# Kernel tuning notes

Measured on AMD Instinct MI355X. Metric: run time of the kernel, lower is better.

The kernel has to match this reference:

```python
import jax, jax.numpy as jnp
import numpy as np

T, B, D_IN, H = 256, 64, 512, 1024  # cell hidden = 2*H
D_OUT = 512
CH = 2 * H  # GRUCell hidden size


def setup_inputs() -> dict:
    key = jax.random.key(0)
    ks = jax.random.split(key, 12)
    s = 0.02
    x = jax.random.normal(ks[0], (T, B, D_IN), dtype=jnp.float32)
    # enc: Linear(D_IN, H)
    We = jax.random.normal(ks[1], (H, D_IN), dtype=jnp.float32) * s
    be = jnp.zeros((H,), dtype=jnp.float32)
    # GRUCell(H, CH): weight_ih [3*CH, H], weight_hh [3*CH, CH]
    Wih = jax.random.normal(ks[2], (3 * CH, H), dtype=jnp.float32) * s
    bih = jnp.zeros((3 * CH,), dtype=jnp.float32)
    Whh = jax.random.normal(ks[3], (3 * CH, CH), dtype=jnp.float32) * s
    bhh = jnp.zeros((3 * CH,), dtype=jnp.float32)
    # heads: Linear(H, D_OUT)
    Wmu = jax.random.normal(ks[4], (D_OUT, H), dtype=jnp.float32) * s
    bmu = jnp.zeros((D_OUT,), dtype=jnp.float32)
    Wsig = jax.random.normal(ks[5], (D_OUT, H), dtype=jnp.float32) * s
    bsig = jnp.zeros((D_OUT,), dtype=jnp.float32)
    return {"x": x, "We": We, "be": be, "Wih": Wih, "bih": bih,
            "Whh": Whh, "bhh": bhh, "Wmu": Wmu, "bmu": bmu,
            "Wsig": Wsig, "bsig": bsig}


def _forward(x, We, be, Wih, bih, Whh, bhh, Wmu, bmu, Wsig, bsig):
    # encode every timestep at once: [T,B,H]
    xe = jax.nn.elu(jnp.einsum('tbd,hd->tbh', x, We) + be)
    # precompute input-side gate preactivations: [T,B,3*CH]
    gx = jnp.einsum('tbh,gh->tbg', xe, Wih) + bih

    def step(h, gx_t):
        gh = h @ Whh.T + bhh                      # [B, 3*CH]
        xr, xz, xn = jnp.split(gx_t, 3, axis=-1)
        hr, hz, hn = jnp.split(gh, 3, axis=-1)
        r = jax.nn.sigmoid(xr + hr)
        z = jax.nn.sigmoid(xz + hz)
        n = jnp.tanh(xn + r * hn)
        h_new = (1.0 - z) * n + z * h
        return h_new, h_new

    h0 = jnp.zeros((x.shape[1], CH), dtype=x.dtype)
    _, hidden = jax.lax.scan(step, h0, gx)        # hidden: [T, B, 2H]

    h_mu, h_sig = jnp.split(hidden, 2, axis=2)    # each [T, B, H]
    mu = jax.nn.elu(jnp.einsum('tbh,oh->tbo', h_mu, Wmu) + bmu)
    sig = jax.nn.softplus(jnp.einsum('tbh,oh->tbo', h_sig, Wsig) + bsig) + 0.1
    return mu, sig, hidden


def reference(x, We, be, Wih, bih, Whh, bhh, Wmu, bmu, Wsig, bsig):
    # Returns (mu, sig, hidden); the torch module wraps (mu, sig) in Normal.
    return _forward(x, We, be, Wih, bih, Whh, bhh, Wmu, bmu, Wsig, bsig)
```

## Files before the change

kernel.cpp:

```cpp
#include <hip/hip_runtime.h>
#include <hip/hip_bf16.h>
#include <math.h>

#define T_STEPS 256
#define B_SZ 64
#define DIN 512
#define H_SZ 1024
#define CH_SZ 2048
#define G3 6144
#define DOUT 512
#define TB 16384

typedef __attribute__((ext_vector_type(4))) float f32x4;
typedef __attribute__((ext_vector_type(8))) short s16x8;
typedef __attribute__((ext_vector_type(4))) short s16x4;
typedef __attribute__((ext_vector_type(4))) unsigned u32x4;
typedef __attribute__((ext_vector_type(8))) __bf16 bf16x8;

__device__ __forceinline__ unsigned short f2bf(float f) {
  unsigned u = __builtin_bit_cast(unsigned, f);
  u += 0x7fffu + ((u >> 16) & 1u);
  return (unsigned short)(u >> 16);
}
__device__ __forceinline__ float bf2f(unsigned short h) {
  unsigned u = ((unsigned)h) << 16;
  return __builtin_bit_cast(float, u);
}
__device__ __forceinline__ f32x4 mfma16(s16x8 a, s16x8 b, f32x4 c) {
  return __builtin_amdgcn_mfma_f32_16x16x32_bf16(
      __builtin_bit_cast(bf16x8, a), __builtin_bit_cast(bf16x8, b), c, 0, 0, 0);
}
__device__ __forceinline__ s16x8 cvt8(f32x4 lo, f32x4 hi) {
  unsigned r0, r1, r2, r3;
  asm("v_cvt_pk_bf16_f32 %0, %1, %2" : "=v"(r0) : "v"(lo.x), "v"(lo.y));
  asm("v_cvt_pk_bf16_f32 %0, %1, %2" : "=v"(r1) : "v"(lo.z), "v"(lo.w));
  asm("v_cvt_pk_bf16_f32 %0, %1, %2" : "=v"(r2) : "v"(hi.x), "v"(hi.y));
  asm("v_cvt_pk_bf16_f32 %0, %1, %2" : "=v"(r3) : "v"(hi.z), "v"(hi.w));
  u32x4 p; p[0] = r0; p[1] = r1; p[2] = r2; p[3] = r3;
  return __builtin_bit_cast(s16x8, p);
}

template<bool AF32, int ACT, bool OBF>
__global__ __launch_bounds__(256, 2)
void gemm_bt(const void* __restrict__ Ap, long lda,
             const unsigned short* __restrict__ Bp,
             const float* __restrict__ bias,
             float* __restrict__ Cf, unsigned short* __restrict__ Cb, long ldc,
             int K)
{
  __shared__ unsigned short sA[128 * 40];
  __shared__ unsigned short sB[128 * 40];
  const int tid  = threadIdx.x;
  const int lane = tid & 63;
  const int wave = tid >> 6;
  const int wm = wave & 1, wn = wave >> 1;
  const int l16 = lane & 15, quad = lane >> 4;
  const long m0 = (long)blockIdx.x * 128;
  const long n0 = (long)blockIdx.y * 128;
  const int srow = tid >> 1;
  const int sseg = (tid & 1) << 4;

  f32x4 acc[4][4] = {};

  for (int k0 = 0; k0 < K; k0 += 32) {
    if constexpr (AF32) {
      const float* A = (const float*)Ap + (m0 + srow) * lda + (k0 + sseg);
      f32x4 v0 = *(const f32x4*)(A + 0);
      f32x4 v1 = *(const f32x4*)(A + 4);
      f32x4 v2 = *(const f32x4*)(A + 8);
      f32x4 v3 = *(const f32x4*)(A + 12);
      s16x8 p0, p1;
      p0[0] = (short)f2bf(v0.x); p0[1] = (short)f2bf(v0.y);
      p0[2] = (short)f2bf(v0.z); p0[3] = (short)f2bf(v0.w);
      p0[4] = (short)f2bf(v1.x); p0[5] = (short)f2bf(v1.y);
      p0[6] = (short)f2bf(v1.z); p0[7] = (short)f2bf(v1.w);
      p1[0] = (short)f2bf(v2.x); p1[1] = (short)f2bf(v2.y);
      p1[2] = (short)f2bf(v2.z); p1[3] = (short)f2bf(v2.w);
      p1[4] = (short)f2bf(v3.x); p1[5] = (short)f2bf(v3.y);
      p1[6] = (short)f2bf(v3.z); p1[7] = (short)f2bf(v3.w);
      *(s16x8*)&sA[srow * 40 + sseg]     = p0;
      *(s16x8*)&sA[srow * 40 + sseg + 8] = p1;
    } else {
      const unsigned short* A = (const unsigned short*)Ap + (m0 + srow) * lda + (k0 + sseg);
      *(s16x8*)&sA[srow * 40 + sseg]     = *(const s16x8*)(A);
      *(s16x8*)&sA[srow * 40 + sseg + 8] = *(const s16x8*)(A + 8);
    }
    {
      const unsigned short* Bq = Bp + (n0 + srow) * (long)K + (k0 + sseg);
      *(s16x8*)&sB[srow * 40 + sseg]     = *(const s16x8*)(Bq);
      *(s16x8*)&sB[srow * 40 + sseg + 8] = *(const s16x8*)(Bq + 8);
    }
    __syncthreads();
    s16x8 af[4], bfr[4];
#pragma unroll
    for (int i = 0; i < 4; ++i) {
      af[i]  = *(const s16x8*)&sA[(wm * 64 + i * 16 + l16) * 40 + quad * 8];
      bfr[i] = *(const s16x8*)&sB[(wn * 64 + i * 16 + l16) * 40 + quad * 8];
    }
#pragma unroll
    for (int mi = 0; mi < 4; ++mi)
#pragma unroll
      for (int ni = 0; ni < 4; ++ni)
        acc[mi][ni] = mfma16(af[mi], bfr[ni], acc[mi][ni]);
    __syncthreads();
  }

#pragma unroll
  for (int mi = 0; mi < 4; ++mi) {
#pragma unroll
    for (int ni = 0; ni < 4; ++ni) {
      const long n = n0 + wn * 64 + ni * 16 + l16;
      const float bv = bias[n];
#pragma unroll
      for (int i = 0; i < 4; ++i) {
        const long m = m0 + wm * 64 + mi * 16 + quad * 4 + i;
        float v = acc[mi][ni][i] + bv;
        if constexpr (ACT == 1) v = v > 0.f ? v : expm1f(v);
        if constexpr (ACT == 2) v = fmaxf(v, 0.f) + log1pf(expf(-fabsf(v))) + 0.1f;
        if constexpr (OBF) Cb[m * ldc + n] = f2bf(v);
        else               Cf[m * ldc + n] = v;
      }
    }
  }
}

#define GRU_BLOCKS 256
#define UPB 8
#define WROWS 24
#define WSTR 2050

__global__ __launch_bounds__(512, 2)
void gru_persist(const unsigned short* __restrict__ gxb,
                 const float* __restrict__ Whh,
                 const float* __restrict__ bhh,
                 float* hid,
                 unsigned* sy)
{
  __shared__ unsigned short sW[WROWS * WSTR];
  __shared__ float scr[8][24][17];
  const int tid  = threadIdx.x;
  const int lane = tid & 63;
  const int wave = tid >> 6;
  const int l16  = lane & 15, quad = lane >> 4;
  const int bt   = wave & 3;
  const int kh   = wave >> 2;
  const int jb   = blockIdx.x * UPB;

  for (int wr = 0; wr < WROWS; ++wr) {
    const int gate = wr >> 3, u = wr & 7;
    const float* src = Whh + (long)(gate * CH_SZ + jb + u) * CH_SZ + tid * 4;
    f32x4 v = *(const f32x4*)src;
    s16x4 p;
    p[0] = (short)f2bf(v.x); p[1] = (short)f2bf(v.y);
    p[2] = (short)f2bf(v.z); p[3] = (short)f2bf(v.w);
    *(s16x4*)&sW[wr * WSTR + tid * 4] = p;
  }

  const int om  = tid >> 3;
  const int ou  = tid & 7;
  const int oj  = jb + ou;
  const int obt = om >> 4, omi = om & 15;
  const float br_ = bhh[oj], bz_ = bhh[CH_SZ + oj], bn_ = bhh[2 * CH_SZ + oj];

  const unsigned short* w0 = &sW[l16 * WSTR + kh * 1024 + quad * 8];
  const unsigned short* w1 = &sW[(16 + (l16 & 7)) * WSTR + kh * 1024 + quad * 8];

  float ho = 0.f;
  __syncthreads();

  for (int t = 0; t < T_STEPS; ++t) {
    const unsigned short* gxt = gxb + (long)t * (B_SZ * G3) + (long)om * G3 + oj;
    const unsigned short gxr = gxt[0];
    const unsigned short gxz = gxt[CH_SZ];
    const unsigned short gxn = gxt[2 * CH_SZ];

    if (t > 0) {
      const float* hb = hid + (long)(t - 1) * (B_SZ * CH_SZ)
                            + (long)(bt * 16 + l16) * CH_SZ + kh * 1024 + quad * 8;
      f32x4 a0 = {}, a1 = {};
      f32x4 P[8], Q[8];
#pragma unroll
      for (int u = 0; u < 4; ++u) {
        P[2 * u]     = *(const f32x4*)(hb + u * 32);
        P[2 * u + 1] = *(const f32x4*)(hb + u * 32 + 4);
      }
#pragma unroll
      for (int c = 0; c < 8; ++c) {
        f32x4* CUR = (c & 1) ? Q : P;
        f32x4* NXT = (c & 1) ? P : Q;
        if (c < 7) {
#pragma unroll
          for (int u = 0; u < 4; ++u) {
            NXT[2 * u]     = *(const f32x4*)(hb + ((c + 1) * 4 + u) * 32);
            NXT[2 * u + 1] = *(const f32x4*)(hb + ((c + 1) * 4 + u) * 32 + 4);
          }
        }
#pragma unroll
        for (int u = 0; u < 4; ++u) {
          const int s = c * 4 + u;
          s16x8 af = cvt8(CUR[2 * u], CUR[2 * u + 1]);
          a0 = mfma16(af, *(const s16x8*)(w0 + s * 32), a0);
          a1 = mfma16(af, *(const s16x8*)(w1 + s * 32), a1);
        }
      }
#pragma unroll
      for (int i = 0; i < 4; ++i) scr[wave][l16][quad * 4 + i] = a0[i];
      if (l16 < 8) {
#pragma unroll
        for (int i = 0; i < 4; ++i) scr[wave][16 + l16][quad * 4 + i] = a1[i];
      }
    }
    __syncthreads();

    float ghr = 0.f, ghz = 0.f, ghn = 0.f;
    if (t > 0) {
      ghr = scr[obt][ou][omi]      + scr[4 + obt][ou][omi];
      ghz = scr[obt][8 + ou][omi]  + scr[4 + obt][8 + ou][omi];
      ghn = scr[obt][16 + ou][omi] + scr[4 + obt][16 + ou][omi];
    }
    const float xr = bf2f(gxr), xz = bf2f(gxz), xn = bf2f(gxn);
    const float r = 1.f / (1.f + expf(-(xr + ghr + br_)));
    const float z = 1.f / (1.f + expf(-(xz + ghz + bz_)));
    const float n = tanhf(xn + r * (ghn + bn_));
    const float hv = (1.f - z) * n + z * ho;
    ho = hv;
    atomicExch(&hid[(long)t * (B_SZ * CH_SZ) + (long)om * CH_SZ + oj], hv);

    if (t < T_STEPS - 1) {
      __syncthreads();
      const unsigned tv = (unsigned)(t + 1);
      if (blockIdx.x == 0) {
        if (tid >= 1 && tid < 256) {
          while (__hip_atomic_load(&sy[tid * 16], __ATOMIC_RELAXED,
                                   __HIP_MEMORY_SCOPE_AGENT) < tv)
            __builtin_amdgcn_s_sleep(1);
        }
        __syncthreads();
        if (tid < 8) atomicExch(&sy[(256 + tid) * 16], tv);
      } else {
        if (tid == 0) {
          atomicExch(&sy[blockIdx.x * 16], tv);
          while (__hip_atomic_load(&sy[(256 + (blockIdx.x & 7)) * 16],
                                   __ATOMIC_RELAXED, __HIP_MEMORY_SCOPE_AGENT) < tv)
            __builtin_amdgcn_s_sleep(1);
        }
        __syncthreads();
      }
      asm volatile("" ::: "memory");
    }
  }
}

__global__ void cast_f32_bf16(const float* __restrict__ s, unsigned short* __restrict__ d, long n) {
  long i = ((long)blockIdx.x * blockDim.x + threadIdx.x) * 4;
  if (i + 3 < n) {
    f32x4 v = *(const f32x4*)(s + i);
    s16x4 p;
    p[0] = (short)f2bf(v.x); p[1] = (short)f2bf(v.y);
    p[2] = (short)f2bf(v.z); p[3] = (short)f2bf(v.w);
    *(s16x4*)(d + i) = p;
  }
}

__global__ void zero_u32(unsigned int* p, int n) {
  int i = blockIdx.x * blockDim.x + threadIdx.x;
  if (i < n) p[i] = 0u;
}

extern "C" void kernel_launch(void* const* d_in, const int* in_sizes, int n_in,
                              void* d_out, int out_size, void* d_ws, size_t ws_size,
                              hipStream_t stream)
{
  const float* x    = (const float*)d_in[0];
  const float* We   = (const float*)d_in[1];
  const float* be   = (const float*)d_in[2];
  const float* Wih  = (const float*)d_in[3];
  const float* bih  = (const float*)d_in[4];
  const float* Whh  = (const float*)d_in[5];
  const float* bhh  = (const float*)d_in[6];
  const float* Wmu  = (const float*)d_in[7];
  const float* bmu  = (const float*)d_in[8];
  const float* Wsig = (const float*)d_in[9];
  const float* bsig = (const float*)d_in[10];

  float* out = (float*)d_out;
  float* mu  = out;
  float* sg  = out + (long)TB * DOUT;
  float* hid = out + 2L * TB * DOUT;

  char* w = (char*)d_ws;
  unsigned short* Web  = (unsigned short*)w; w += (long)H_SZ * DIN * 2;
  unsigned short* Wihb = (unsigned short*)w; w += (long)G3 * H_SZ * 2;
  unsigned short* Wmub = (unsigned short*)w; w += (long)DOUT * H_SZ * 2;
  unsigned short* Wsgb = (unsigned short*)w; w += (long)DOUT * H_SZ * 2;
  unsigned short* xeb  = (unsigned short*)w; w += (long)TB * H_SZ * 2;
  unsigned short* gxb  = (unsigned short*)w; w += (long)TB * G3 * 2;
  unsigned*       sy   = (unsigned*)w;       w += 272 * 16 * 4;

  auto cast = [&](const float* s, unsigned short* d, long n) {
    int blocks = (int)((n / 4 + 255) / 256);
    cast_f32_bf16<<<blocks, 256, 0, stream>>>(s, d, n);
  };
  cast(We,   Web,  (long)H_SZ * DIN);
  cast(Wih,  Wihb, (long)G3 * H_SZ);
  cast(Wmu,  Wmub, (long)DOUT * H_SZ);
  cast(Wsig, Wsgb, (long)DOUT * H_SZ);
  zero_u32<<<17, 256, 0, stream>>>((unsigned int*)sy, 272 * 16);

  gemm_bt<true, 1, true><<<dim3(TB / 128, H_SZ / 128), 256, 0, stream>>>(
      x, (long)DIN, Web, be, nullptr, xeb, (long)H_SZ, DIN);

  gemm_bt<false, 0, true><<<dim3(TB / 128, G3 / 128), 256, 0, stream>>>(
      xeb, (long)H_SZ, Wihb, bih, nullptr, gxb, (long)G3, H_SZ);

  {
    void* kargs[] = {
      (void*)&gxb, (void*)&Whh, (void*)&bhh, (void*)&hid, (void*)&sy
    };
    hipLaunchCooperativeKernel((void*)gru_persist, dim3(GRU_BLOCKS), dim3(512),
                               kargs, 0, stream);
  }

  gemm_bt<true, 1, false><<<dim3(TB / 128, DOUT / 128), 256, 0, stream>>>(
      hid, (long)CH_SZ, Wmub, bmu, mu, nullptr, (long)DOUT, H_SZ);
  gemm_bt<true, 2, false><<<dim3(TB / 128, DOUT / 128), 256, 0, stream>>>(
      hid + H_SZ, (long)CH_SZ, Wsgb, bsig, sg, nullptr, (long)DOUT, H_SZ);
}
```

Before: 5.505 ms.

## Publish bf16 hidden copy, use flat all-to-all barrier, prefetch next gate inputs

The GRU recurrence now writes a packed bf16 copy of each hidden state to a workspace buffer with coherent atomics, and the next step's matvec reads that copy instead of the fp32 hidden. This halves the bytes read per step and drops the per-element conversions. The fp32 hidden output becomes a plain store. The two-level barrier through block 0 is replaced by a flat one where every block polls all 256 flags, and the next step's gx values are loaded before the wait. This trades a shorter barrier critical path for more polling traffic, and relies on the plain stores becoming visible without atomics.

```diff
diff --git a/kernel.cpp b/kernel.cpp
--- a/kernel.cpp
+++ b/kernel.cpp
@@ -14,7 +14,6 @@
 typedef __attribute__((ext_vector_type(4))) float f32x4;
 typedef __attribute__((ext_vector_type(8))) short s16x8;
 typedef __attribute__((ext_vector_type(4))) short s16x4;
-typedef __attribute__((ext_vector_type(4))) unsigned u32x4;
 typedef __attribute__((ext_vector_type(8))) __bf16 bf16x8;
 
 __device__ __forceinline__ unsigned short f2bf(float f) {
@@ -29,15 +28,6 @@
 __device__ __forceinline__ f32x4 mfma16(s16x8 a, s16x8 b, f32x4 c) {
   return __builtin_amdgcn_mfma_f32_16x16x32_bf16(
       __builtin_bit_cast(bf16x8, a), __builtin_bit_cast(bf16x8, b), c, 0, 0, 0);
-}
-__device__ __forceinline__ s16x8 cvt8(f32x4 lo, f32x4 hi) {
-  unsigned r0, r1, r2, r3;
-  asm("v_cvt_pk_bf16_f32 %0, %1, %2" : "=v"(r0) : "v"(lo.x), "v"(lo.y));
-  asm("v_cvt_pk_bf16_f32 %0, %1, %2" : "=v"(r1) : "v"(lo.z), "v"(lo.w));
-  asm("v_cvt_pk_bf16_f32 %0, %1, %2" : "=v"(r2) : "v"(hi.x), "v"(hi.y));
-  asm("v_cvt_pk_bf16_f32 %0, %1, %2" : "=v"(r3) : "v"(hi.z), "v"(hi.w));
-  u32x4 p; p[0] = r0; p[1] = r1; p[2] = r2; p[3] = r3;
-  return __builtin_bit_cast(s16x8, p);
 }
 
 template<bool AF32, int ACT, bool OBF>
@@ -134,6 +124,7 @@
                  const float* __restrict__ Whh,
                  const float* __restrict__ bhh,
                  float* hid,
+                 unsigned short* hxb,
                  unsigned* sy)
 {
   __shared__ unsigned short sW[WROWS * WSTR];
@@ -166,41 +157,35 @@
   const unsigned short* w1 = &sW[(16 + (l16 & 7)) * WSTR + kh * 1024 + quad * 8];
 
   float ho = 0.f;
+  unsigned short gxr, gxz, gxn;
+  {
+    const unsigned short* g0 = gxb + (long)om * G3 + oj;
+    gxr = g0[0]; gxz = g0[CH_SZ]; gxn = g0[2 * CH_SZ];
+  }
   __syncthreads();
 
   for (int t = 0; t < T_STEPS; ++t) {
-    const unsigned short* gxt = gxb + (long)t * (B_SZ * G3) + (long)om * G3 + oj;
-    const unsigned short gxr = gxt[0];
-    const unsigned short gxz = gxt[CH_SZ];
-    const unsigned short gxn = gxt[2 * CH_SZ];
-
     if (t > 0) {
-      const float* hb = hid + (long)(t - 1) * (B_SZ * CH_SZ)
-                            + (long)(bt * 16 + l16) * CH_SZ + kh * 1024 + quad * 8;
+      const unsigned short* hb = hxb + (long)(t - 1) * (B_SZ * CH_SZ)
+                               + (long)(bt * 16 + l16) * CH_SZ + kh * 1024 + quad * 8;
+      s16x8 P[8], Q[8];
       f32x4 a0 = {}, a1 = {};
-      f32x4 P[8], Q[8];
-#pragma unroll
-      for (int u = 0; u < 4; ++u) {
-        P[2 * u]     = *(const f32x4*)(hb + u * 32);
-        P[2 * u + 1] = *(const f32x4*)(hb + u * 32 + 4);
-      }
-#pragma unroll
-      for (int c = 0; c < 8; ++c) {
-        f32x4* CUR = (c & 1) ? Q : P;
-        f32x4* NXT = (c & 1) ? P : Q;
-        if (c < 7) {
-#pragma unroll
-          for (int u = 0; u < 4; ++u) {
-            NXT[2 * u]     = *(const f32x4*)(hb + ((c + 1) * 4 + u) * 32);
-            NXT[2 * u + 1] = *(const f32x4*)(hb + ((c + 1) * 4 + u) * 32 + 4);
-          }
+#pragma unroll
+      for (int u = 0; u < 8; ++u) P[u] = *(const s16x8*)(hb + u * 32);
+#pragma unroll
+      for (int c = 0; c < 4; ++c) {
+        s16x8* CUR = (c & 1) ? Q : P;
+        s16x8* NXT = (c & 1) ? P : Q;
+        if (c < 3) {
+#pragma unroll
+          for (int u = 0; u < 8; ++u)
+            NXT[u] = *(const s16x8*)(hb + ((c + 1) * 8 + u) * 32);
         }
 #pragma unroll
-        for (int u = 0; u < 4; ++u) {
-          const int s = c * 4 + u;
-          s16x8 af = cvt8(CUR[2 * u], CUR[2 * u + 1]);
-          a0 = mfma16(af, *(const s16x8*)(w0 + s * 32), a0);
-          a1 = mfma16(af, *(const s16x8*)(w1 + s * 32), a1);
+        for (int u = 0; u < 8; ++u) {
+          const int s = c * 8 + u;
+          a0 = mfma16(CUR[u], *(const s16x8*)(w0 + s * 32), a0);
+          a1 = mfma16(CUR[u], *(const s16x8*)(w1 + s * 32), a1);
         }
       }
 #pragma unroll
@@ -224,29 +209,29 @@
     const float n = tanhf(xn + r * (ghn + bn_));
     const float hv = (1.f - z) * n + z * ho;
     ho = hv;
-    atomicExch(&hid[(long)t * (B_SZ * CH_SZ) + (long)om * CH_SZ + oj], hv);
+    hid[(long)t * (B_SZ * CH_SZ) + (long)om * CH_SZ + oj] = hv;
+
+    const float hvn = __shfl_down(hv, 1);
+    if ((lane & 1) == 0) {
+      unsigned pk;
+      asm("v_cvt_pk_bf16_f32 %0, %1, %2" : "=v"(pk) : "v"(hv), "v"(hvn));
+      atomicExch((unsigned*)(hxb + (long)t * (B_SZ * CH_SZ) + (long)om * CH_SZ + oj), pk);
+    }
 
     if (t < T_STEPS - 1) {
       __syncthreads();
       const unsigned tv = (unsigned)(t + 1);
-      if (blockIdx.x == 0) {
-        if (tid >= 1 && tid < 256) {
-          while (__hip_atomic_load(&sy[tid * 16], __ATOMIC_RELAXED,
-                                   __HIP_MEMORY_SCOPE_AGENT) < tv)
-            __builtin_amdgcn_s_sleep(1);
-        }
-        __syncthreads();
-        if (tid < 8) atomicExch(&sy[(256 + tid) * 16], tv);
-      } else {
-        if (tid == 0) {
-          atomicExch(&sy[blockIdx.x * 16], tv);
-          while (__hip_atomic_load(&sy[(256 + (blockIdx.x & 7)) * 16],
-                                   __ATOMIC_RELAXED, __HIP_MEMORY_SCOPE_AGENT) < tv)
-            __builtin_amdgcn_s_sleep(1);
-        }
-        __syncthreads();
+      if (tid == 0) atomicExch(&sy[blockIdx.x * 16], tv);
+      const unsigned short* g1 = gxb + (long)tv * (B_SZ * G3) + (long)om * G3 + oj;
+      const unsigned short nr = g1[0], nz = g1[CH_SZ], nn = g1[2 * CH_SZ];
+      if (tid < 256) {
+        while (__hip_atomic_load(&sy[tid * 16], __ATOMIC_RELAXED,
+                                 __HIP_MEMORY_SCOPE_AGENT) < tv)
+          __builtin_amdgcn_s_sleep(2);
       }
+      __syncthreads();
       asm volatile("" ::: "memory");
+      gxr = nr; gxz = nz; gxn = nn;
     }
   }
 }
@@ -295,6 +280,7 @@
   unsigned short* Wsgb = (unsigned short*)w; w += (long)DOUT * H_SZ * 2;
   unsigned short* xeb  = (unsigned short*)w; w += (long)TB * H_SZ * 2;
   unsigned short* gxb  = (unsigned short*)w; w += (long)TB * G3 * 2;
+  unsigned short* hxb  = (unsigned short*)w; w += (long)T_STEPS * B_SZ * CH_SZ * 2;
   unsigned*       sy   = (unsigned*)w;       w += 272 * 16 * 4;
 
   auto cast = [&](const float* s, unsigned short* d, long n) {
@@ -315,7 +301,7 @@
 
   {
     void* kargs[] = {
-      (void*)&gxb, (void*)&Whh, (void*)&bhh, (void*)&hid, (void*)&sy
+      (void*)&gxb, (void*)&Whh, (void*)&bhh, (void*)&hid, (void*)&hxb, (void*)&sy
     };
     hipLaunchCooperativeKernel((void*)gru_persist, dim3(GRU_BLOCKS), dim3(512),
                                kargs, 0, stream);
```

New measurement: 5.163 ms. 6.2% less time.
